# Performance work log

Hardware: AMD Instinct MI355X
Metric: run time of the kernel (lower is better)

The kernel has to match this reference:

```python
import jax, jax.numpy as jnp
import numpy as np

B, S, D, H = 4, 2048, 1024, 16
HD = D // H


def setup_inputs() -> dict:
    key = jax.random.key(0)
    ks = jax.random.split(key, 5)
    s_in = 1.0 / np.sqrt(D)
    return {
        "x": jax.random.normal(ks[0], (B, S, D), dtype=jnp.float32),
        "W_attn": jax.random.uniform(ks[1], (D, 3 * D), dtype=jnp.float32, minval=-s_in, maxval=s_in),
        "b_attn": jax.random.uniform(ks[2], (3 * D,), dtype=jnp.float32, minval=-s_in, maxval=s_in),
        "W_proj": jax.random.uniform(ks[3], (D, D), dtype=jnp.float32, minval=-s_in, maxval=s_in),
        "b_proj": jax.random.uniform(ks[4], (D,), dtype=jnp.float32, minval=-s_in, maxval=s_in),
    }


def reference(x, W_attn, b_attn, W_proj, b_proj):
    b, s, d = x.shape
    qkv = x @ W_attn + b_attn                      # [B,S,3D]
    q, k, v = jnp.split(qkv, 3, axis=-1)
    # [B,H,S,HD]
    q = q.reshape(b, s, H, HD).transpose(0, 2, 1, 3)
    k = k.reshape(b, s, H, HD).transpose(0, 2, 1, 3)
    v = v.reshape(b, s, H, HD).transpose(0, 2, 1, 3)
    scale = 1.0 / np.sqrt(HD)
    att = jnp.einsum("bhqd,bhkd->bhqk", q, k) * scale
    causal = jnp.tril(jnp.ones((s, s), dtype=bool))
    att = jnp.where(causal[None, None], att, -jnp.inf)
    att = jax.nn.softmax(att, axis=-1)
    y = jnp.einsum("bhqk,bhkd->bhqd", att, v)      # [B,H,S,HD]
    y = y.transpose(0, 2, 1, 3).reshape(b, s, d)
    return y @ W_proj + b_proj
```

## Files before the change

### kernel.cpp

```cpp
#include <hip/hip_runtime.h>

#define B_  4
#define S_  2048
#define D_  1024
#define H_  16
#define HD_ 64
#define BS_ (B_*S_)

typedef _Float16 f16;
typedef _Float16 f16_8 __attribute__((ext_vector_type(8)));
typedef _Float16 f16_4 __attribute__((ext_vector_type(4)));
typedef float    f32_4 __attribute__((ext_vector_type(4)));
typedef unsigned int u32;

#define MFMA32(a,b,c) __builtin_amdgcn_mfma_f32_16x16x32_f16(a, b, c, 0, 0, 0)
#define MFMA16(a,b,c) __builtin_amdgcn_mfma_f32_16x16x16f16(a, b, c, 0, 0, 0)
#define NEG_INF (-__builtin_inff())

__device__ inline void gl_lds16(const f16* g, f16* lds_base, int chunk_base) {
    __builtin_amdgcn_global_load_lds(
        (const __attribute__((address_space(1))) u32*)g,
        (__attribute__((address_space(3))) u32*)(lds_base + (size_t)chunk_base * 8),
        16, 0, 0);
}

__global__ __launch_bounds__(256) void prep(
    const float* __restrict__ X,  f16* __restrict__ Xh,
    const float* __restrict__ Wa, f16* __restrict__ Wta)
{
    __shared__ f16 T[64][72];
    const int t = threadIdx.x;
    const int bid = blockIdx.x;
    if (bid < 4096) {
        const size_t i = ((size_t)bid * 256 + t) * 8;
        float4 a = *(const float4*)&X[i];
        float4 b = *(const float4*)&X[i + 4];
        f16 h[8] = {(f16)a.x,(f16)a.y,(f16)a.z,(f16)a.w,
                    (f16)b.x,(f16)b.y,(f16)b.z,(f16)b.w};
        *(uint4*)&Xh[i] = *(const uint4*)h;
        return;
    }
    const int idx = bid - 4096;
    const int n0 = (idx % 48) * 64, k0 = (idx / 48) * 64;
    const int nl4 = (t & 15) * 4;
    #pragma unroll
    for (int r = 0; r < 4; r++) {
        const int kl = (t >> 4) + r * 16;
        float4 v = *(const float4*)&Wa[(size_t)(k0 + kl) * 3072 + n0 + nl4];
        T[nl4 + 0][kl] = (f16)v.x;
        T[nl4 + 1][kl] = (f16)v.y;
        T[nl4 + 2][kl] = (f16)v.z;
        T[nl4 + 3][kl] = (f16)v.w;
    }
    __syncthreads();
    const int nr = t >> 2, kc = (t & 3) * 16;
    *(uint4*)&Wta[(size_t)(n0 + nr) * 1024 + k0 + kc]     = *(uint4*)&T[nr][kc];
    *(uint4*)&Wta[(size_t)(n0 + nr) * 1024 + k0 + kc + 8] = *(uint4*)&T[nr][kc + 8];
}

__global__ __launch_bounds__(256) void trans_w(
    const float* __restrict__ W, f16* __restrict__ Wt, int ncols)
{
    __shared__ f16 T[64][72];
    const int t = threadIdx.x;
    const int n0 = blockIdx.x * 64, k0 = blockIdx.y * 64;
    const int nl4 = (t & 15) * 4;
    #pragma unroll
    for (int r = 0; r < 4; r++) {
        const int kl = (t >> 4) + r * 16;
        float4 v = *(const float4*)&W[(size_t)(k0 + kl) * ncols + n0 + nl4];
        T[nl4 + 0][kl] = (f16)v.x;
        T[nl4 + 1][kl] = (f16)v.y;
        T[nl4 + 2][kl] = (f16)v.z;
        T[nl4 + 3][kl] = (f16)v.w;
    }
    __syncthreads();
    const int nr = t >> 2, kc = (t & 3) * 16;
    *(uint4*)&Wt[(size_t)(n0 + nr) * 1024 + k0 + kc]     = *(uint4*)&T[nr][kc];
    *(uint4*)&Wt[(size_t)(n0 + nr) * 1024 + k0 + kc + 8] = *(uint4*)&T[nr][kc + 8];
}

__global__ __launch_bounds__(256) void qkv_gemm(
    const f16*   __restrict__ Xh,
    const f16*   __restrict__ Wta,
    const float* __restrict__ bias,
    f16* __restrict__ Qb, f16* __restrict__ Kb, f16* __restrict__ Vt)
{
    __shared__ f16 lds[17408];
    f16* Af[2] = {lds,        lds + 4096};
    f16* Bf[2] = {lds + 8192, lds + 12288};
    f16* Ct    = lds;

    const int t    = threadIdx.x;
    const int lane = t & 63;
    const int w    = t >> 6;
    const int quad = lane >> 4, l15 = lane & 15;
    const int wr = w >> 1, wc = w & 1;
    const int m0 = blockIdx.x * 128;
    const int n0 = blockIdx.y * 128;
    const int wbase = t & 192;

    f32_4 acc[4][4] = {};

    for (int k0 = 0; k0 < 1024; k0 += 64) {
        #pragma unroll
        for (int kc = 0; kc < 2; kc++)
            #pragma unroll
            for (int c = 0; c < 2; c++) {
                int i = c*256 + t;
                const int row = i >> 2, col = (i & 3) * 8;
                gl_lds16(Xh  + (size_t)(m0 + row)*1024 + k0 + kc*32 + col,
                         Af[kc], c*256 + wbase);
                gl_lds16(Wta + (size_t)(n0 + row)*1024 + k0 + kc*32 + col,
                         Bf[kc], c*256 + wbase);
            }
        __syncthreads();

        #pragma unroll
        for (int kc = 0; kc < 2; kc++) {
            f16_8 af[4], bf[4];
            #pragma unroll
            for (int mi = 0; mi < 4; mi++)
                af[mi] = *(const f16_8*)&Af[kc][(wr*64 + mi*16 + l15)*32 + quad*8];
            #pragma unroll
            for (int ni = 0; ni < 4; ni++)
                bf[ni] = *(const f16_8*)&Bf[kc][(wc*64 + ni*16 + l15)*32 + quad*8];
            #pragma unroll
            for (int mi = 0; mi < 4; mi++)
                #pragma unroll
                for (int ni = 0; ni < 4; ni++)
                    acc[mi][ni] = MFMA32(af[mi], bf[ni], acc[mi][ni]);
        }
        __syncthreads();
    }

    const int which = n0 >> 10;
    float bcol[4];
    #pragma unroll
    for (int ni = 0; ni < 4; ni++)
        bcol[ni] = bias[n0 + wc*64 + ni*16 + l15];

    if (which < 2) {
        f16* dst = (which == 0) ? Qb : Kb;
        const float sc = (which == 0) ? 0.125f * 1.44269504f : 1.0f;
        #pragma unroll
        for (int mi = 0; mi < 4; mi++)
        #pragma unroll
        for (int ni = 0; ni < 4; ni++)
        #pragma unroll
        for (int r = 0; r < 4; r++) {
            int m = m0 + wr*64 + mi*16 + quad*4 + r;
            int n = (n0 & 1023) + wc*64 + ni*16 + l15;
            int h = n >> 6, hd = n & 63;
            int b = m >> 11, s = m & 2047;
            dst[((size_t)(b*16 + h)*2048 + s)*64 + hd] =
                (f16)((acc[mi][ni][r] + bcol[ni]) * sc);
        }
    } else {
        #pragma unroll
        for (int mi = 0; mi < 4; mi++)
        #pragma unroll
        for (int ni = 0; ni < 4; ni++)
        #pragma unroll
        for (int r = 0; r < 4; r++) {
            int nl = wc*64 + ni*16 + l15;
            int ml = wr*64 + mi*16 + quad*4 + r;
            Ct[nl*136 + ml] = (f16)(acc[mi][ni][r] + bcol[ni]);
        }
        __syncthreads();
        const int row = t >> 1, sc4 = (t & 1) * 64;
        const int n = (n0 & 1023) + row;
        const int h = n >> 6, hd = n & 63;
        const int b = m0 >> 11, s0 = (m0 & 2047) + sc4;
        f16* dst = Vt + ((size_t)(b*16 + h)*64 + hd)*2048 + s0;
        #pragma unroll
        for (int j = 0; j < 8; j++)
            *(uint4*)&dst[j*8] = *(uint4*)&Ct[row*136 + sc4 + j*8];
    }
}

__global__ __launch_bounds__(256) void attn(
    const f16* __restrict__ Qb,
    const f16* __restrict__ Kb,
    const f16* __restrict__ Vt,
    f16* __restrict__ Y)
{
    __shared__ f16 Ks[64*72];
    __shared__ f16 Vs[64*72];

    const int t    = threadIdx.x;
    const int w    = t >> 6;
    const int lane = t & 63;
    const int quad = lane >> 4, l15 = lane & 15;
    const int bh   = blockIdx.x;
    const int b    = bh >> 4, h = bh & 15;

    const f16* qh = Qb + (size_t)bh * S_ * 64;
    const f16* kh = Kb + (size_t)bh * S_ * 64;
    const f16* vt = Vt + (size_t)bh * 64 * S_;

    const int sk = t >> 2, sc = (t & 3) * 8;
    const f16_4 ones = {(f16)1,(f16)1,(f16)1,(f16)1};

    #pragma unroll 1
    for (int sp = 0; sp < 2; sp++) {
        const int qb = sp ? 15 - (int)blockIdx.y : (int)blockIdx.y;
        const int qw = qb*128 + w*32;

        f16_8 qa[2][2];
        #pragma unroll
        for (int rt = 0; rt < 2; rt++)
            #pragma unroll
            for (int c = 0; c < 2; c++)
                qa[rt][c] = *(const f16_8*)&qh[(size_t)(qw + rt*16 + l15)*64 + c*32 + quad*8];

        f32_4 o[2][4] = {};
        f32_4 lacc[2] = {};
        const int ntiles = 2*qb + 2;

        for (int kt = 0; kt < ntiles; kt++) {
            const int kbase = kt * 64;
            *(uint4*)&Ks[sk*72 + sc]      = *(const uint4*)&kh[(size_t)(kbase + sk)*64 + sc];
            *(uint4*)&Ks[sk*72 + sc + 32] = *(const uint4*)&kh[(size_t)(kbase + sk)*64 + sc + 32];
            *(uint4*)&Vs[sk*72 + sc]      = *(const uint4*)&vt[(size_t)sk*2048 + kbase + sc];
            *(uint4*)&Vs[sk*72 + sc + 32] = *(const uint4*)&vt[(size_t)sk*2048 + kbase + sc + 32];
            __syncthreads();

            if (kbase <= qw + 31) {
                f16_8 kb[4][2];
                #pragma unroll
                for (int sub = 0; sub < 4; sub++)
                    #pragma unroll
                    for (int c = 0; c < 2; c++)
                        kb[sub][c] = *(const f16_8*)&Ks[(sub*16 + l15)*72 + c*32 + quad*8];
                f32_4 st[2][4];
                #pragma unroll
                for (int rt = 0; rt < 2; rt++)
                    #pragma unroll
                    for (int sub = 0; sub < 4; sub++) {
                        f32_4 a = {};
                        a = MFMA32(kb[sub][0], qa[rt][0], a);
                        a = MFMA32(kb[sub][1], qa[rt][1], a);
                        st[rt][sub] = a;
                    }

                const bool masked = (kbase + 63 > qw);
                f16_4 pt[2][4];
                #pragma unroll
                for (int rt = 0; rt < 2; rt++)
                #pragma unroll
                for (int sub = 0; sub < 4; sub++) {
                    const int qrow = qw + rt*16 + l15;
                    f16_4 p;
                    #pragma unroll
                    for (int r = 0; r < 4; r++) {
                        float x = st[rt][sub][r];
                        if (masked) {
                            int key = kbase + sub*16 + quad*4 + r;
                            x = (key <= qrow) ? x : NEG_INF;
                        }
                        p[r] = (f16)__builtin_amdgcn_exp2f(x);
                    }
                    pt[rt][sub] = p;
                }

                #pragma unroll
                for (int rt = 0; rt < 2; rt++) {
                    f16_4 ps = (pt[rt][0] + pt[rt][1]) + (pt[rt][2] + pt[rt][3]);
                    lacc[rt] = MFMA16(ps, ones, lacc[rt]);
                }

                #pragma unroll
                for (int sub = 0; sub < 4; sub++) {
                    f16_4 vb[4];
                    #pragma unroll
                    for (int tt = 0; tt < 4; tt++)
                        vb[tt] = *(const f16_4*)&Vs[(tt*16 + l15)*72 + sub*16 + quad*4];
                    #pragma unroll
                    for (int rt = 0; rt < 2; rt++)
                        #pragma unroll
                        for (int tt = 0; tt < 4; tt++)
                            o[rt][tt] = MFMA16(pt[rt][sub], vb[tt], o[rt][tt]);
                }
            }
            __syncthreads();
        }

        #pragma unroll
        for (int rt = 0; rt < 2; rt++)
        #pragma unroll
        for (int r = 0; r < 4; r++) {
            float inv = 1.0f / lacc[rt][r];
            int srow = qw + rt*16 + quad*4 + r;
            #pragma unroll
            for (int tt = 0; tt < 4; tt++)
                Y[(size_t)(b*S_ + srow)*1024 + h*64 + tt*16 + l15] =
                    (f16)(o[rt][tt][r] * inv);
        }
    }
}

__global__ __launch_bounds__(256) void proj_gemm(
    const f16* __restrict__ Yb,
    const f16* __restrict__ Wtp,
    const float* __restrict__ bias,
    float* __restrict__ Out)
{
    __shared__ f16 lds2[16384];
    f16* Af[2] = {lds2,        lds2 + 4096};
    f16* Bf[2] = {lds2 + 8192, lds2 + 12288};

    const int t    = threadIdx.x;
    const int lane = t & 63;
    const int w    = t >> 6;
    const int quad = lane >> 4, l15 = lane & 15;
    const int wr = w >> 1, wc = w & 1;
    const int m0 = blockIdx.x * 128;
    const int n0 = blockIdx.y * 128;
    const int wbase = t & 192;

    f32_4 acc[4][4] = {};

    for (int k0 = 0; k0 < 1024; k0 += 64) {
        #pragma unroll
        for (int kc = 0; kc < 2; kc++)
            #pragma unroll
            for (int c = 0; c < 2; c++) {
                int i = c*256 + t;
                const int row = i >> 2, col = (i & 3) * 8;
                gl_lds16(Yb  + (size_t)(m0 + row)*1024 + k0 + kc*32 + col,
                         Af[kc], c*256 + wbase);
                gl_lds16(Wtp + (size_t)(n0 + row)*1024 + k0 + kc*32 + col,
                         Bf[kc], c*256 + wbase);
            }
        __syncthreads();
        #pragma unroll
        for (int kc = 0; kc < 2; kc++) {
            f16_8 af[4], bf[4];
            #pragma unroll
            for (int mi = 0; mi < 4; mi++)
                af[mi] = *(const f16_8*)&Af[kc][(wr*64 + mi*16 + l15)*32 + quad*8];
            #pragma unroll
            for (int ni = 0; ni < 4; ni++)
                bf[ni] = *(const f16_8*)&Bf[kc][(wc*64 + ni*16 + l15)*32 + quad*8];
            #pragma unroll
            for (int mi = 0; mi < 4; mi++)
                #pragma unroll
                for (int ni = 0; ni < 4; ni++)
                    acc[mi][ni] = MFMA32(af[mi], bf[ni], acc[mi][ni]);
        }
        __syncthreads();
    }

    #pragma unroll
    for (int mi = 0; mi < 4; mi++)
    #pragma unroll
    for (int ni = 0; ni < 4; ni++)
    #pragma unroll
    for (int r = 0; r < 4; r++) {
        int m = m0 + wr*64 + mi*16 + quad*4 + r;
        int n = n0 + wc*64 + ni*16 + l15;
        Out[(size_t)m*1024 + n] = acc[mi][ni][r] + bias[n];
    }
}

extern "C" void kernel_launch(void* const* d_in, const int* in_sizes, int n_in,
                              void* d_out, int out_size, void* d_ws, size_t ws_size,
                              hipStream_t stream) {
    const float* x      = (const float*)d_in[0];
    const float* W_attn = (const float*)d_in[1];
    const float* b_attn = (const float*)d_in[2];
    const float* W_proj = (const float*)d_in[3];
    const float* b_proj = (const float*)d_in[4];
    float* out = (float*)d_out;

    const size_t per = (size_t)B_ * H_ * S_ * HD_;
    f16* Yb  = (f16*)d_ws;
    f16* Wta = Yb;
    f16* Qb  = Yb + per;
    f16* Kb  = Qb + per;
    f16* Vt  = Kb + per;
    f16* Wtp = Qb;
    f16* Xh  = (f16*)d_out;

    prep     <<<4096 + 768, 256, 0, stream>>>(x, Xh, W_attn, Wta);
    qkv_gemm <<<dim3(64, 24), 256, 0, stream>>>(Xh, Wta, b_attn, Qb, Kb, Vt);
    attn     <<<dim3(64, 8),  256, 0, stream>>>(Qb, Kb, Vt, Yb);
    trans_w  <<<dim3(16, 16), 256, 0, stream>>>(W_proj, Wtp, D_);
    proj_gemm<<<dim3(64, 8),  256, 0, stream>>>(Yb, Wtp, b_proj, out);
}
```

Before: 269.7 us.

## Restructure QKV GEMM into 128x256 triple-buffered swizzled LDS pipeline

The QKV projection GEMM now uses 512-thread blocks computing 128x256 output tiles. It triple-buffers 64-wide K tiles in LDS with XOR-swizzled layouts, loaded asynchronously with global_load_lds. The B-tile loads are split into two halves interleaved with MFMA phases, with raised wave priority during the MFMAs, so global-to-LDS transfers overlap compute and LDS bank conflicts drop. The cost is a much larger LDS footprint, which limits blocks per CU, and fewer blocks in the grid.

```diff
diff --git a/kernel.cpp b/kernel.cpp
--- a/kernel.cpp
+++ b/kernel.cpp
@@ -80,58 +80,132 @@
     *(uint4*)&Wt[(size_t)(n0 + nr) * 1024 + k0 + kc + 8] = *(uint4*)&T[nr][kc + 8];
 }
 
-__global__ __launch_bounds__(256) void qkv_gemm(
+__global__ __launch_bounds__(512, 2) void qkv_gemm(
     const f16*   __restrict__ Xh,
     const f16*   __restrict__ Wta,
     const float* __restrict__ bias,
     f16* __restrict__ Qb, f16* __restrict__ Kb, f16* __restrict__ Vt)
 {
-    __shared__ f16 lds[17408];
-    f16* Af[2] = {lds,        lds + 4096};
-    f16* Bf[2] = {lds + 8192, lds + 12288};
-    f16* Ct    = lds;
+    __shared__ f16 lds[73728];
 
     const int t    = threadIdx.x;
     const int lane = t & 63;
     const int w    = t >> 6;
     const int quad = lane >> 4, l15 = lane & 15;
-    const int wr = w >> 1, wc = w & 1;
+    const int wr = w >> 2, wc = w & 3;
     const int m0 = blockIdx.x * 128;
-    const int n0 = blockIdx.y * 128;
-    const int wbase = t & 192;
+    const int n0 = blockIdx.y * 256;
+    const int wb = t & 448;
+
+    int aoff[2], boff[4];
+    #pragma unroll
+    for (int c = 0; c < 2; c++) {
+        const int i = c*512 + t, row = i >> 3, sl = i & 7;
+        aoff[c] = row*1024 + ((sl ^ (row & 7)) << 3);
+    }
+    #pragma unroll
+    for (int c = 0; c < 4; c++) {
+        const int i = c*512 + t, row = i >> 3, sl = i & 7;
+        boff[c] = row*1024 + ((sl ^ (row & 7)) << 3);
+    }
+    int fa[4][2], fb[4][2];
+    #pragma unroll
+    for (int mi = 0; mi < 4; mi++)
+        #pragma unroll
+        for (int kk = 0; kk < 2; kk++)
+            fa[mi][kk] = (wr*64 + mi*16 + l15)*64 + (((kk*4 + quad) ^ (l15 & 7)) << 3);
+    #pragma unroll
+    for (int ni = 0; ni < 4; ni++)
+        #pragma unroll
+        for (int kk = 0; kk < 2; kk++)
+            fb[ni][kk] = (wc*64 + ni*16 + l15)*64 + (((kk*4 + quad) ^ (l15 & 7)) << 3);
+
+    const f16* Ag = Xh  + (size_t)m0 * 1024;
+    const f16* Bg = Wta + (size_t)n0 * 1024;
 
     f32_4 acc[4][4] = {};
 
-    for (int k0 = 0; k0 < 1024; k0 += 64) {
-        #pragma unroll
-        for (int kc = 0; kc < 2; kc++)
-            #pragma unroll
-            for (int c = 0; c < 2; c++) {
-                int i = c*256 + t;
-                const int row = i >> 2, col = (i & 3) * 8;
-                gl_lds16(Xh  + (size_t)(m0 + row)*1024 + k0 + kc*32 + col,
-                         Af[kc], c*256 + wbase);
-                gl_lds16(Wta + (size_t)(n0 + row)*1024 + k0 + kc*32 + col,
-                         Bf[kc], c*256 + wbase);
-            }
-        __syncthreads();
-
-        #pragma unroll
-        for (int kc = 0; kc < 2; kc++) {
-            f16_8 af[4], bf[4];
+    #pragma unroll
+    for (int c = 0; c < 2; c++) gl_lds16(Ag + aoff[c],       lds,                c*512 + wb);
+    #pragma unroll
+    for (int c = 0; c < 4; c++) gl_lds16(Bg + boff[c],       lds + 8192,         c*512 + wb);
+    #pragma unroll
+    for (int c = 0; c < 2; c++) gl_lds16(Ag + 64 + aoff[c],  lds + 24576,        c*512 + wb);
+    #pragma unroll
+    for (int c = 0; c < 4; c++) gl_lds16(Bg + 64 + boff[c],  lds + 24576 + 8192, c*512 + wb);
+    asm volatile("s_waitcnt vmcnt(6)" ::: "memory");
+    __builtin_amdgcn_s_barrier();
+    asm volatile("" ::: "memory");
+
+    int cur = 0;
+    #pragma unroll 1
+    for (int T = 0; T < 16; T++) {
+        f16* buf        = lds + cur*24576;
+        const int nxt   = cur ? cur - 1 : 2;
+        f16* nbuf       = lds + nxt*24576;
+        const bool st   = (T < 14);
+        const int  kt2  = (T + 2) * 64;
+
+        if (st) {
+            #pragma unroll
+            for (int c = 0; c < 2; c++)
+                gl_lds16(Ag + kt2 + aoff[c], nbuf, c*512 + wb);
+        }
+        f16_8 af[4][2], bf[2][2];
+        #pragma unroll
+        for (int mi = 0; mi < 4; mi++)
+            #pragma unroll
+            for (int kk = 0; kk < 2; kk++)
+                af[mi][kk] = *(const f16_8*)&buf[fa[mi][kk]];
+        #pragma unroll
+        for (int ni = 0; ni < 2; ni++)
+            #pragma unroll
+            for (int kk = 0; kk < 2; kk++)
+                bf[ni][kk] = *(const f16_8*)&buf[8192 + fb[ni][kk]];
+        asm volatile("" ::: "memory");
+        __builtin_amdgcn_s_barrier();
+        asm volatile("" ::: "memory");
+        __builtin_amdgcn_s_setprio(1);
+        #pragma unroll
+        for (int kk = 0; kk < 2; kk++)
             #pragma unroll
             for (int mi = 0; mi < 4; mi++)
-                af[mi] = *(const f16_8*)&Af[kc][(wr*64 + mi*16 + l15)*32 + quad*8];
-            #pragma unroll
-            for (int ni = 0; ni < 4; ni++)
-                bf[ni] = *(const f16_8*)&Bf[kc][(wc*64 + ni*16 + l15)*32 + quad*8];
+                #pragma unroll
+                for (int ni = 0; ni < 2; ni++)
+                    acc[mi][ni] = MFMA32(af[mi][kk], bf[ni][kk], acc[mi][ni]);
+        __builtin_amdgcn_s_setprio(0);
+        asm volatile("" ::: "memory");
+        __builtin_amdgcn_s_barrier();
+        asm volatile("" ::: "memory");
+
+        if (st) {
+            #pragma unroll
+            for (int c = 0; c < 4; c++)
+                gl_lds16(Bg + kt2 + boff[c], nbuf + 8192, c*512 + wb);
+        }
+        #pragma unroll
+        for (int ni = 0; ni < 2; ni++)
+            #pragma unroll
+            for (int kk = 0; kk < 2; kk++)
+                bf[ni][kk] = *(const f16_8*)&buf[8192 + fb[2 + ni][kk]];
+        asm volatile("" ::: "memory");
+        __builtin_amdgcn_s_barrier();
+        asm volatile("" ::: "memory");
+        __builtin_amdgcn_s_setprio(1);
+        #pragma unroll
+        for (int kk = 0; kk < 2; kk++)
             #pragma unroll
             for (int mi = 0; mi < 4; mi++)
                 #pragma unroll
-                for (int ni = 0; ni < 4; ni++)
-                    acc[mi][ni] = MFMA32(af[mi], bf[ni], acc[mi][ni]);
-        }
-        __syncthreads();
+                for (int ni = 0; ni < 2; ni++)
+                    acc[mi][2 + ni] = MFMA32(af[mi][kk], bf[ni][kk], acc[mi][2 + ni]);
+        __builtin_amdgcn_s_setprio(0);
+        if (T < 14)       asm volatile("s_waitcnt vmcnt(6)" ::: "memory");
+        else if (T == 14) asm volatile("s_waitcnt vmcnt(0)" ::: "memory");
+        __builtin_amdgcn_s_barrier();
+        asm volatile("" ::: "memory");
+
+        cur = (cur >= 2) ? 0 : cur + 1;
     }
 
     const int which = n0 >> 10;
@@ -157,6 +231,7 @@
                 (f16)((acc[mi][ni][r] + bcol[ni]) * sc);
         }
     } else {
+        f16* Ct = lds;
         #pragma unroll
         for (int mi = 0; mi < 4; mi++)
         #pragma unroll
@@ -168,14 +243,15 @@
             Ct[nl*136 + ml] = (f16)(acc[mi][ni][r] + bcol[ni]);
         }
         __syncthreads();
-        const int row = t >> 1, sc4 = (t & 1) * 64;
-        const int n = (n0 & 1023) + row;
-        const int h = n >> 6, hd = n & 63;
-        const int b = m0 >> 11, s0 = (m0 & 2047) + sc4;
+        const int row = t >> 1, half = t & 1;
+        const int nv = (n0 & 1023) + row;
+        const int h = nv >> 6, hd = nv & 63;
+        const int b = m0 >> 11;
+        const int s0 = (m0 & 2047) + half*64;
         f16* dst = Vt + ((size_t)(b*16 + h)*64 + hd)*2048 + s0;
         #pragma unroll
         for (int j = 0; j < 8; j++)
-            *(uint4*)&dst[j*8] = *(uint4*)&Ct[row*136 + sc4 + j*8];
+            *(uint4*)&dst[j*8] = *(uint4*)&Ct[row*136 + half*64 + j*8];
     }
 }
 
@@ -384,7 +460,7 @@
     f16* Xh  = (f16*)d_out;
 
     prep     <<<4096 + 768, 256, 0, stream>>>(x, Xh, W_attn, Wta);
-    qkv_gemm <<<dim3(64, 24), 256, 0, stream>>>(Xh, Wta, b_attn, Qb, Kb, Vt);
+    qkv_gemm <<<dim3(64, 12), 512, 0, stream>>>(Xh, Wta, b_attn, Qb, Kb, Vt);
     attn     <<<dim3(64, 8),  256, 0, stream>>>(Qb, Kb, Vt, Yb);
     trans_w  <<<dim3(16, 16), 256, 0, stream>>>(W_proj, Wtp, D_);
     proj_gemm<<<dim3(64, 8),  256, 0, stream>>>(Yb, Wtp, b_proj, out);
```

Result: no change. 273.5 us (+1.4%).
